# Kernel tuning notes

Hardware: AMD Instinct MI355X
Metric: run time of the kernel (lower is better)

The kernel has to match this reference:

```python
import jax, jax.numpy as jnp
import numpy as np

T_REFRAC = 2  # t_refrac init kwarg


def setup_inputs() -> dict:
    key = jax.random.key(0)
    B, T, N = 16, 256, 8192
    x = jax.random.uniform(key, (B, T, N), dtype=jnp.float32)
    return {"x": x}


def reference(x) -> jnp.ndarray:
    """SpikingCell with track_spikes, enable_clamp, t_refrac=2, buffer_dv,
    reset_mechanism='subtract', accumulate_only=False.
    Concrete hooks: _compute_dv = identity, _count_spikes = sum over features.
    Keras RNN initializes all states to zeros.
    Returns the per-timestep spike outputs [B, T, N]."""
    B, T, N = x.shape
    v0 = jnp.zeros((B, N), x.dtype)        # membrane potential
    sc0 = jnp.zeros((B,), x.dtype)         # spike counter
    clamp0 = jnp.zeros((B,), x.dtype)      # clamp countdown
    refrac0 = jnp.zeros((B, N), x.dtype)   # refractory counters
    buf0 = jnp.zeros((B, N), x.dtype)      # one-step dv buffer

    def step(carry, x_t):
        v, sc, clamp, refrac, dv_buf = carry
        dv = x_t  # _compute_dv = identity
        # buffer_dv: integrate previous step's dv
        dvi = dv_buf
        # _filter_update: clamp gate (layer-global per batch) then refractory gate
        dvi = dvi * (clamp[:, None] <= 0.0).astype(dvi.dtype)
        dvi = dvi * (refrac >= T_REFRAC).astype(dvi.dtype)
        v = v + dvi
        out = (v >= 1.0).astype(v.dtype)
        v = v - out  # reset by subtraction
        sc = sc + jnp.sum(x_t, axis=-1)  # _count_spikes = sum over features
        clamp = clamp - 1.0
        refrac = (refrac + 1.0) * (out == 0.0).astype(refrac.dtype)
        return (v, sc, clamp, refrac, dv), out

    x_tbn = jnp.transpose(x, (1, 0, 2))  # [T, B, N]
    _, outs = jax.lax.scan(step, (v0, sc0, clamp0, refrac0, buf0), x_tbn)
    return jnp.transpose(outs, (1, 0, 2))  # [B, T, N]
```

## Files before the change

### kernel.cpp

```cpp
#include <hip/hip_runtime.h>


constexpr int B = 16;
constexpr int T = 256;
constexpr int N = 8192;
constexpr int U = 16;

__global__ __launch_bounds__(256, 2) void spiking_kernel(
    const float* __restrict__ x, float* __restrict__ out) {
  const int c = blockIdx.x * blockDim.x + threadIdx.x;
  const int b = c >> 13;
  const int n = c & (N - 1);

  const float* __restrict__ xp = x + (size_t)b * T * N + n;
  float* __restrict__ op = out + (size_t)b * T * N + n;

  float v = 0.f, refrac = 0.f, buf = 0.f;

  float cur[U], nxt[U];

#pragma unroll
  for (int u = 0; u < U; ++u) cur[u] = xp[(size_t)u * N];

  for (int g = 0; g < T / U - 1; ++g) {
    const size_t base_next = (size_t)(g + 1) * U * N;
#pragma unroll
    for (int u = 0; u < U; ++u) nxt[u] = xp[base_next + (size_t)u * N];

    const size_t base_cur = (size_t)g * U * N;
#pragma unroll
    for (int u = 0; u < U; ++u) {
      const float dvi = (refrac >= 2.0f) ? buf : 0.0f;
      v += dvi;
      const float o = (v >= 1.0f) ? 1.0f : 0.0f;
      v -= o;
      refrac = (o == 0.0f) ? (refrac + 1.0f) : 0.0f;
      buf = cur[u];
      op[base_cur + (size_t)u * N] = o;
    }

#pragma unroll
    for (int u = 0; u < U; ++u) cur[u] = nxt[u];
  }

  const size_t base_last = (size_t)(T - U) * N;
#pragma unroll
  for (int u = 0; u < U; ++u) {
    const float dvi = (refrac >= 2.0f) ? buf : 0.0f;
    v += dvi;
    const float o = (v >= 1.0f) ? 1.0f : 0.0f;
    v -= o;
    refrac = (o == 0.0f) ? (refrac + 1.0f) : 0.0f;
    buf = cur[u];
    op[base_last + (size_t)u * N] = o;
  }
}

extern "C" void kernel_launch(void* const* d_in, const int* in_sizes, int n_in,
                              void* d_out, int out_size, void* d_ws,
                              size_t ws_size, hipStream_t stream) {
  const float* x = (const float*)d_in[0];
  float* out = (float*)d_out;

  const int threads = 256;
  const int total = B * N;
  const int blocks = total / threads;
  spiking_kernel<<<blocks, threads, 0, stream>>>(x, out);
}
```

Before: 232.3 us.

## Double-buffer input chunks in LDS via async global-to-LDS loads

Input timesteps are now prefetched with global_load_lds into two shared-memory buffers that alternate by chunk, instead of being held in register arrays. Each wave loads its own 64-element slice, so no block barrier is needed. The aim is to free registers and overlap the next chunk's loads with the sequential recurrence and the stores. It relies on the compiler inserting correct vmcnt waits before the LDS reads; those waits may also stall on outstanding stores.

Result: slower. 237.7 us (+2.3%).

```diff
diff --git a/kernel.cpp b/kernel.cpp
--- a/kernel.cpp
+++ b/kernel.cpp
@@ -1,58 +1,85 @@
 #include <hip/hip_runtime.h>
+#include <stdint.h>
 
 
 constexpr int B = 16;
 constexpr int T = 256;
 constexpr int N = 8192;
-constexpr int U = 16;
+constexpr int CH = 16;
+constexpr int BLK = 256;
+constexpr int NG = T / CH;
 
-__global__ __launch_bounds__(256, 2) void spiking_kernel(
+typedef __attribute__((address_space(3))) uint32_t lds_u32;
+typedef __attribute__((address_space(1))) const uint32_t glb_u32;
+
+__global__ __launch_bounds__(BLK) void spiking_kernel(
     const float* __restrict__ x, float* __restrict__ out) {
-  const int c = blockIdx.x * blockDim.x + threadIdx.x;
-  const int b = c >> 13;
-  const int n = c & (N - 1);
+  __shared__ float sA[CH][BLK];
+  __shared__ float sB[CH][BLK];
+
+  const int tid = threadIdx.x;
+  const int gid = blockIdx.x * BLK + tid;
+  const int b = gid >> 13;
+  const int n = gid & (N - 1);
+  const int wbase = (tid >> 6) * 64;
 
   const float* __restrict__ xp = x + (size_t)b * T * N + n;
   float* __restrict__ op = out + (size_t)b * T * N + n;
 
   float v = 0.f, refrac = 0.f, buf = 0.f;
 
-  float cur[U], nxt[U];
-
 #pragma unroll
-  for (int u = 0; u < U; ++u) cur[u] = xp[(size_t)u * N];
-
-  for (int g = 0; g < T / U - 1; ++g) {
-    const size_t base_next = (size_t)(g + 1) * U * N;
-#pragma unroll
-    for (int u = 0; u < U; ++u) nxt[u] = xp[base_next + (size_t)u * N];
-
-    const size_t base_cur = (size_t)g * U * N;
-#pragma unroll
-    for (int u = 0; u < U; ++u) {
-      const float dvi = (refrac >= 2.0f) ? buf : 0.0f;
-      v += dvi;
-      const float o = (v >= 1.0f) ? 1.0f : 0.0f;
-      v -= o;
-      refrac = (o == 0.0f) ? (refrac + 1.0f) : 0.0f;
-      buf = cur[u];
-      op[base_cur + (size_t)u * N] = o;
-    }
-
-#pragma unroll
-    for (int u = 0; u < U; ++u) cur[u] = nxt[u];
+  for (int u = 0; u < CH; ++u) {
+    __builtin_amdgcn_global_load_lds((glb_u32*)(xp + (size_t)u * N),
+                                     (lds_u32*)&sA[u][wbase], 4, 0, 0);
   }
 
-  const size_t base_last = (size_t)(T - U) * N;
+#pragma unroll 1
+  for (int g = 0; g < NG; g += 2) {
+    {
+      const size_t tb = (size_t)(g + 1) * CH;
 #pragma unroll
-  for (int u = 0; u < U; ++u) {
-    const float dvi = (refrac >= 2.0f) ? buf : 0.0f;
-    v += dvi;
-    const float o = (v >= 1.0f) ? 1.0f : 0.0f;
-    v -= o;
-    refrac = (o == 0.0f) ? (refrac + 1.0f) : 0.0f;
-    buf = cur[u];
-    op[base_last + (size_t)u * N] = o;
+      for (int u = 0; u < CH; ++u) {
+        __builtin_amdgcn_global_load_lds((glb_u32*)(xp + (tb + u) * N),
+                                         (lds_u32*)&sB[u][wbase], 4, 0, 0);
+      }
+    }
+    {
+      const size_t ob = (size_t)g * CH;
+#pragma unroll
+      for (int u = 0; u < CH; ++u) {
+        const float xt = sA[u][tid];
+        const float dvi = (refrac >= 2.0f) ? buf : 0.0f;
+        v += dvi;
+        const float o = (v >= 1.0f) ? 1.0f : 0.0f;
+        v -= o;
+        refrac = (o == 0.0f) ? (refrac + 1.0f) : 0.0f;
+        buf = xt;
+        op[(ob + u) * N] = o;
+      }
+    }
+    if (g + 2 < NG) {
+      const size_t tb = (size_t)(g + 2) * CH;
+#pragma unroll
+      for (int u = 0; u < CH; ++u) {
+        __builtin_amdgcn_global_load_lds((glb_u32*)(xp + (tb + u) * N),
+                                         (lds_u32*)&sA[u][wbase], 4, 0, 0);
+      }
+    }
+    {
+      const size_t ob = (size_t)(g + 1) * CH;
+#pragma unroll
+      for (int u = 0; u < CH; ++u) {
+        const float xt = sB[u][tid];
+        const float dvi = (refrac >= 2.0f) ? buf : 0.0f;
+        v += dvi;
+        const float o = (v >= 1.0f) ? 1.0f : 0.0f;
+        v -= o;
+        refrac = (o == 0.0f) ? (refrac + 1.0f) : 0.0f;
+        buf = xt;
+        op[(ob + u) * N] = o;
+      }
+    }
   }
 }
 
@@ -62,8 +89,7 @@
   const float* x = (const float*)d_in[0];
   float* out = (float*)d_out;
 
-  const int threads = 256;
   const int total = B * N;
-  const int blocks = total / threads;
-  spiking_kernel<<<blocks, threads, 0, stream>>>(x, out);
+  const int blocks = total / BLK;
+  spiking_kernel<<<blocks, BLK, 0, stream>>>(x, out);
 }
```
